# Performance work log

Measured on AMD Instinct MI355X. Metric: run time of the kernel, lower is better.

Reference implementation:

```python
import jax, jax.numpy as jnp
import numpy as np

N_HEAD = 4
GROUPS = 32
EPS = 1e-5


def group_norm(x, scale, bias):
    B, C, H, W = x.shape
    xg = x.reshape(B, GROUPS, C // GROUPS, H, W)
    mu = xg.mean(axis=(2, 3, 4), keepdims=True)
    var = xg.var(axis=(2, 3, 4), keepdims=True)
    xg = (xg - mu) * jax.lax.rsqrt(var + EPS)
    x = xg.reshape(B, C, H, W)
    return x * scale[None, :, None, None] + bias[None, :, None, None]


def setup_inputs() -> dict:
    key = jax.random.key(0)
    k0, k1, k2 = jax.random.split(key, 3)
    B, C, H, W = 2, 64, 64, 64
    x = jax.random.normal(k0, (B, C, H, W), dtype=jnp.float32)
    gn_scale = jnp.ones((C,), dtype=jnp.float32)
    gn_bias = jnp.zeros((C,), dtype=jnp.float32)
    w_qkv = jax.random.normal(k1, (3 * C, C), dtype=jnp.float32) * 0.05  # 1x1 conv, no bias
    w_out = jax.random.normal(k2, (C, C), dtype=jnp.float32) * 0.05     # 1x1 conv
    b_out = jnp.zeros((C,), dtype=jnp.float32)
    return {"x": x, "gn_scale": gn_scale, "gn_bias": gn_bias,
            "w_qkv": w_qkv, "w_out": w_out, "b_out": b_out}


def reference(x, gn_scale, gn_bias, w_qkv, w_out, b_out):
    B, C, H, W = x.shape
    head_dim = C // N_HEAD
    norm = group_norm(x, gn_scale, gn_bias)
    # 1x1 conv == channel matmul
    qkv = jnp.einsum('oc,bchw->bohw', w_qkv, norm)
    qkv = qkv.reshape(B, N_HEAD, head_dim * 3, H, W)
    q, k, v = jnp.split(qkv, 3, axis=2)  # each [B, n, head_dim, H, W]
    # full spatial attention scores, scaled by sqrt(channel) as in source
    attn = jnp.einsum('bnchw,bncyx->bnhwyx', q, k) / jnp.sqrt(jnp.float32(C))
    attn = jax.nn.softmax(attn.reshape(B, N_HEAD, H, W, H * W), axis=-1)
    attn = attn.reshape(B, N_HEAD, H, W, H, W)
    out = jnp.einsum('bnhwyx,bncyx->bnchw', attn, v).reshape(B, C, H, W)
    out = jnp.einsum('oc,bchw->bohw', w_out, out) + b_out[None, :, None, None]
    return out + x
```

## Files before the change

### kernel.cpp

```cpp
#include <hip/hip_runtime.h>
#include <hip/hip_bf16.h>

typedef __attribute__((ext_vector_type(8))) short short8;
typedef __attribute__((ext_vector_type(4))) float f32x4;
typedef __attribute__((ext_vector_type(16))) float f32x16;
typedef __attribute__((ext_vector_type(4))) unsigned short ushort4v;
typedef __attribute__((ext_vector_type(4))) unsigned int uint4v;

#define DEV static __device__ __forceinline__

DEV unsigned short f2bf(float f){
  unsigned u = __float_as_uint(f);
  u += 0x7fffu + ((u >> 16) & 1u);
  return (unsigned short)(u >> 16);
}

DEV unsigned pack2bf(float a, float b){
  __hip_bfloat162 h = __float22bfloat162_rn(make_float2(a, b));
  unsigned u;
  __builtin_memcpy(&u, &h, 4);
  return u;
}

#define QSCALE 0.180336880111f

__global__ __launch_bounds__(256) void gn_partial_k(const float* __restrict__ x,
                                                    float* __restrict__ gp){
  int blk = blockIdx.x;
  float4 v = ((const float4*)(x + (size_t)blk*1024))[threadIdx.x];
  float s = v.x+v.y+v.z+v.w;
  float q = v.x*v.x+v.y*v.y+v.z*v.z+v.w*v.w;
  #pragma unroll
  for (int off = 1; off < 64; off <<= 1){
    s += __shfl_xor(s, off);
    q += __shfl_xor(q, off);
  }
  __shared__ float red[8];
  int w = threadIdx.x >> 6;
  if ((threadIdx.x & 63) == 0){ red[w*2] = s; red[w*2+1] = q; }
  __syncthreads();
  if (threadIdx.x == 0){
    gp[blk*2+0] = red[0]+red[2]+red[4]+red[6];
    gp[blk*2+1] = red[1]+red[3]+red[5]+red[7];
  }
}

__global__ __launch_bounds__(256) void qkv_k(const float* __restrict__ x,
    const float* __restrict__ gp, const float* __restrict__ gsc,
    const float* __restrict__ gbi, const float* __restrict__ wq,
    unsigned short* __restrict__ q, unsigned short* __restrict__ k,
    unsigned short* __restrict__ v){
  int b  = blockIdx.x >> 7;
  int s0 = (blockIdx.x & 127) * 32;
  __shared__ float W[192][68];
  __shared__ float A[32][68];
  __shared__ float MS[32][2];
  int t = threadIdx.x;
  for (int i = t; i < 3072; i += 256){
    int o = i >> 4, c4 = (i & 15) * 4;
    *(float4*)&W[o][c4] = ((const float4*)wq)[i];
  }
  if (t < 32){
    float s = 0.f, ss = 0.f;
    #pragma unroll
    for (int i = 0; i < 8; ++i){
      const float* pp = gp + ((b*32 + t)*8 + i)*2;
      s += pp[0]; ss += pp[1];
    }
    float mean = s * (1.f/8192.f);
    MS[t][0] = mean;
    MS[t][1] = rsqrtf(ss * (1.f/8192.f) - mean*mean + 1e-5f);
  }
  __syncthreads();
  {
    int c  = t >> 2;
    int s8 = (t & 3) * 8;
    const float* px = x + ((size_t)b*64 + c)*4096 + s0 + s8;
    float4 v0 = *(const float4*)px;
    float4 v1 = *(const float4*)(px + 4);
    float sc = gsc[c] * MS[c>>1][1];
    float bi = gbi[c] - MS[c>>1][0] * sc;
    A[s8+0][c]=v0.x*sc+bi; A[s8+1][c]=v0.y*sc+bi; A[s8+2][c]=v0.z*sc+bi; A[s8+3][c]=v0.w*sc+bi;
    A[s8+4][c]=v1.x*sc+bi; A[s8+5][c]=v1.y*sc+bi; A[s8+6][c]=v1.z*sc+bi; A[s8+7][c]=v1.w*sc+bi;
  }
  __syncthreads();
  int sl = t >> 3, grp = t & 7;
  float acc[24];
  #pragma unroll
  for (int j = 0; j < 24; ++j) acc[j] = 0.f;
  for (int c4 = 0; c4 < 16; ++c4){
    float4 a = *(const float4*)&A[sl][c4*4];
    #pragma unroll
    for (int j = 0; j < 24; ++j){
      float4 wv = *(const float4*)&W[grp + j*8][c4*4];
      acc[j] = fmaf(a.x, wv.x, fmaf(a.y, wv.y, fmaf(a.z, wv.z, fmaf(a.w, wv.w, acc[j]))));
    }
  }
  int s = s0 + sl;
  #pragma unroll
  for (int j = 0; j < 24; ++j){
    int o = grp + j*8;
    int n = o / 48, r = o % 48;
    size_t base = (((size_t)b*4 + n)*4096 + s)*16;
    float val = acc[j];
    if (r < 16)       q[base + r]      = f2bf(val * QSCALE);
    else if (r < 32)  k[base + r - 16] = f2bf(val);
    else              v[base + r - 32] = f2bf(val);
  }
}

template<int LNSP>
__global__ __launch_bounds__(256) void attn_k(const unsigned short* __restrict__ qb,
    const unsigned short* __restrict__ kb, const unsigned short* __restrict__ vb,
    float* __restrict__ part, float* __restrict__ lsums){
  constexpr int NSP = 1 << LNSP;
  constexpr int NT  = 64 >> LNSP;
  int blk = blockIdx.x;
  int qt = blk & 31;
  int sp = (blk >> 5) & (NSP - 1);
  int bn = blk >> (5 + LNSP);
  int t = threadIdx.x, w = t >> 6, l = t & 63;
  int lq = l & 31, hi = l >> 5;

  const unsigned short* Kp = kb + ((size_t)bn*4096 + sp*(NT*64))*16;
  const unsigned short* Vp = vb + ((size_t)bn*4096 + sp*(NT*64))*16;
  int qrow = qt*128 + w*32;
  const unsigned short* Qp = qb + ((size_t)bn*4096 + qrow)*16;

  __shared__ alignas(16) unsigned short Vt[2][16][72];

  short8 qf = *(const short8*)(Qp + (size_t)lq*16 + hi*8);

  f32x16 O, zero;
  #pragma unroll
  for (int r = 0; r < 16; ++r){ O[r] = 0.f; zero[r] = 0.f; }

  short8 vones;
  #pragma unroll
  for (int r = 0; r < 8; ++r) vones[r] = (short)0x3F80;

  int skv = t >> 2, sd = (t & 3) * 4;
  int xk = skv & 15;
  int scol = (skv & 48) + (xk & 3) + (((xk >> 2) & 1) << 3) + (((xk >> 3) & 1) << 2);
  const unsigned short* vsrc = Vp + (size_t)skv*16 + sd;
  const unsigned short* kaddr = Kp + (size_t)lq*16 + hi*8;

  short8 kf0 = *(const short8*)(kaddr);
  short8 kf1 = *(const short8*)(kaddr + 512);
  {
    ushort4v vv = *(const ushort4v*)(vsrc);
    Vt[0][sd+0][scol]=vv[0]; Vt[0][sd+1][scol]=vv[1];
    Vt[0][sd+2][scol]=vv[2]; Vt[0][sd+3][scol]=vv[3];
  }

  for (int kt = 0; kt < NT; ++kt){
    __syncthreads();
    int cur = kt & 1;
    bool pf = (kt + 1) < NT;
    short8 kn0 = {}, kn1 = {};
    ushort4v vn = {};
    if (pf){
      const unsigned short* ka = kaddr + (size_t)(kt+1)*1024;
      kn0 = *(const short8*)(ka);
      kn1 = *(const short8*)(ka + 512);
      vn  = *(const ushort4v*)(vsrc + (size_t)(kt+1)*1024);
    }

    f32x16 sA = __builtin_amdgcn_mfma_f32_32x32x16_bf16(kf0, qf, zero, 0, 0, 0);
    f32x16 sB = __builtin_amdgcn_mfma_f32_32x32x16_bf16(kf1, qf, zero, 0, 0, 0);

    #pragma unroll
    for (int r = 0; r < 16; ++r) sA[r] = __builtin_amdgcn_exp2f(sA[r]);
    #pragma unroll
    for (int r = 0; r < 16; ++r) sB[r] = __builtin_amdgcn_exp2f(sB[r]);

    auto pvstep = [&](const f32x16& pc, int h8, int vcol){
      uint4v pw;
      pw[0] = pack2bf(pc[h8+0], pc[h8+1]);
      pw[1] = pack2bf(pc[h8+2], pc[h8+3]);
      pw[2] = pack2bf(pc[h8+4], pc[h8+5]);
      pw[3] = pack2bf(pc[h8+6], pc[h8+7]);
      short8 pa = __builtin_bit_cast(short8, pw);
      short8 vf = {};
      if (lq < 16)       vf = *(const short8*)(&Vt[cur][lq][vcol + hi*8]);
      else if (lq == 16) vf = vones;
      O = __builtin_amdgcn_mfma_f32_32x32x16_bf16(pa, vf, O, 0, 0, 0);
    };
    pvstep(sA, 0, 0);
    pvstep(sA, 8, 16);
    pvstep(sB, 0, 32);
    pvstep(sB, 8, 48);

    if (pf){
      Vt[cur^1][sd+0][scol]=vn[0]; Vt[cur^1][sd+1][scol]=vn[1];
      Vt[cur^1][sd+2][scol]=vn[2]; Vt[cur^1][sd+3][scol]=vn[3];
      kf0 = kn0; kf1 = kn1;
    }
  }

  float* Op = part + (((size_t)sp*8 + bn)*4096 + qrow)*16;
  size_t lbase = ((size_t)sp*8 + bn)*4096 + qrow;
  #pragma unroll
  for (int r = 0; r < 16; ++r){
    int qr = (r&3) + 8*(r>>2) + 4*hi;
    if (lq < 16) Op[(size_t)qr*16 + lq] = O[r];
  }
  if (lq == 16){
    #pragma unroll
    for (int r = 0; r < 16; ++r){
      int qr = (r&3) + 8*(r>>2) + 4*hi;
      lsums[lbase + qr] = O[r];
    }
  }
}

__global__ __launch_bounds__(256) void oproj_k(const float* __restrict__ part,
    const float* __restrict__ lsums, const float* __restrict__ wo,
    const float* __restrict__ bo, const float* __restrict__ x,
    float* __restrict__ out, int nsplit){
  int b  = blockIdx.x >> 8;
  int s0 = (blockIdx.x & 255) * 16;
  __shared__ float W[64][68];
  __shared__ float A[16][68];
  int t = threadIdx.x;
  for (int i = t; i < 1024; i += 256){
    int o = i >> 4, c4 = (i & 15) * 4;
    *(float4*)&W[o][c4] = ((const float4*)wo)[i];
  }
  {
    int sl = t & 15;
    int u  = t >> 4;
    int n = u >> 2, d4 = (u & 3) * 4;
    size_t row = ((size_t)b*4 + n)*4096 + s0 + sl;
    float L = 0.f;
    for (int sp = 0; sp < nsplit; ++sp) L += lsums[(size_t)sp*32768 + row];
    float4 acc = {0.f,0.f,0.f,0.f};
    for (int sp = 0; sp < nsplit; ++sp){
      float4 u0 = *(const float4*)(part + ((size_t)sp*32768 + row)*16 + d4);
      acc.x += u0.x; acc.y += u0.y; acc.z += u0.z; acc.w += u0.w;
    }
    float inv = 1.f / L;
    acc.x *= inv; acc.y *= inv; acc.z *= inv; acc.w *= inv;
    *(float4*)&A[sl][n*16 + d4] = acc;
  }
  __syncthreads();
  int sl = t & 15, grp = t >> 4;
  float acc[4] = {0.f,0.f,0.f,0.f};
  for (int c4 = 0; c4 < 16; ++c4){
    float4 a = *(const float4*)&A[sl][c4*4];
    #pragma unroll
    for (int j = 0; j < 4; ++j){
      float4 wv = *(const float4*)&W[grp + j*16][c4*4];
      acc[j] = fmaf(a.x, wv.x, fmaf(a.y, wv.y, fmaf(a.z, wv.z, fmaf(a.w, wv.w, acc[j]))));
    }
  }
  int s = s0 + sl;
  #pragma unroll
  for (int j = 0; j < 4; ++j){
    int o = grp + j*16;
    size_t idx = ((size_t)b*64 + o)*4096 + s;
    out[idx] = acc[j] + bo[o] + x[idx];
  }
}

extern "C" void kernel_launch(void* const* d_in, const int* in_sizes, int n_in,
                              void* d_out, int out_size, void* d_ws, size_t ws_size,
                              hipStream_t stream){
  const float* x   = (const float*)d_in[0];
  const float* gsc = (const float*)d_in[1];
  const float* gbi = (const float*)d_in[2];
  const float* wq  = (const float*)d_in[3];
  const float* wo  = (const float*)d_in[4];
  const float* bo  = (const float*)d_in[5];
  float* out = (float*)d_out;

  char* ws = (char*)d_ws;
  float* gp         = (float*)ws;
  unsigned short* q = (unsigned short*)(ws + 8192);
  unsigned short* k = (unsigned short*)(ws + 8192 + 1048576);
  unsigned short* v = (unsigned short*)(ws + 8192 + 2097152);
  float* part       = (float*)(ws + 8192 + 3145728);

  size_t need8 = 8192 + 3145728 + 8u*2097152 + 8u*131072;
  bool big = ws_size >= need8;
  int nsplit = big ? 8 : 4;
  float* lsums = (float*)(ws + 8192 + 3145728 + (size_t)nsplit*2097152);

  gn_partial_k<<<512,  256, 0, stream>>>(x, gp);
  qkv_k       <<<256,  256, 0, stream>>>(x, gp, gsc, gbi, wq, q, k, v);
  if (big) attn_k<3><<<2048, 256, 0, stream>>>(q, k, v, part, lsums);
  else     attn_k<2><<<1024, 256, 0, stream>>>(q, k, v, part, lsums);
  oproj_k     <<<512,  256, 0, stream>>>(part, lsums, wo, bo, x, out, nsplit);
}
```

Baseline: 61.71 us.

## Reorder attention block mapping, pad V tile with ones row, use nontemporal partials

Remaps block indices so batch-head varies fastest and query tile slowest, which changes L2 locality of K/V across concurrently running blocks. The V shared tile is enlarged to 32 rows with a constant ones row and zero padding, so every lane loads its MFMA operand from LDS instead of branching on the lane index. The V store into LDS moves to the top of the loop, before the barrier. Partial outputs and row sums are written and read with nontemporal hints to avoid polluting cache. The trade-offs are more LDS use, a one-time fill loop, and a barrier ordering that depends on the double-buffer indexing staying correct.

```diff
diff --git a/kernel.cpp b/kernel.cpp
--- a/kernel.cpp
+++ b/kernel.cpp
@@ -116,9 +116,9 @@
   constexpr int NSP = 1 << LNSP;
   constexpr int NT  = 64 >> LNSP;
   int blk = blockIdx.x;
-  int qt = blk & 31;
-  int sp = (blk >> 5) & (NSP - 1);
-  int bn = blk >> (5 + LNSP);
+  int bn = blk & 7;
+  int sp = (blk >> 3) & (NSP - 1);
+  int qt = blk >> (3 + LNSP);
   int t = threadIdx.x, w = t >> 6, l = t & 63;
   int lq = l & 31, hi = l >> 5;
 
@@ -127,17 +127,19 @@
   int qrow = qt*128 + w*32;
   const unsigned short* Qp = qb + ((size_t)bn*4096 + qrow)*16;
 
-  __shared__ alignas(16) unsigned short Vt[2][16][72];
+  __shared__ alignas(16) unsigned short Vt[2][32][72];
+  for (int i = t; i < 2304; i += 256){
+    int buf = (i >= 1152);
+    int ii  = buf ? i - 1152 : i;
+    int row = 16 + ii / 72, col = ii % 72;
+    Vt[buf][row][col] = (row == 16) ? (unsigned short)0x3F80 : (unsigned short)0;
+  }
 
   short8 qf = *(const short8*)(Qp + (size_t)lq*16 + hi*8);
 
   f32x16 O, zero;
   #pragma unroll
   for (int r = 0; r < 16; ++r){ O[r] = 0.f; zero[r] = 0.f; }
-
-  short8 vones;
-  #pragma unroll
-  for (int r = 0; r < 8; ++r) vones[r] = (short)0x3F80;
 
   int skv = t >> 2, sd = (t & 3) * 4;
   int xk = skv & 15;
@@ -147,15 +149,14 @@
 
   short8 kf0 = *(const short8*)(kaddr);
   short8 kf1 = *(const short8*)(kaddr + 512);
-  {
-    ushort4v vv = *(const ushort4v*)(vsrc);
-    Vt[0][sd+0][scol]=vv[0]; Vt[0][sd+1][scol]=vv[1];
-    Vt[0][sd+2][scol]=vv[2]; Vt[0][sd+3][scol]=vv[3];
-  }
+  ushort4v vv = *(const ushort4v*)(vsrc);
 
   for (int kt = 0; kt < NT; ++kt){
+    int cur = kt & 1;
+    Vt[cur][sd+0][scol]=vv[0]; Vt[cur][sd+1][scol]=vv[1];
+    Vt[cur][sd+2][scol]=vv[2]; Vt[cur][sd+3][scol]=vv[3];
     __syncthreads();
-    int cur = kt & 1;
+
     bool pf = (kt + 1) < NT;
     short8 kn0 = {}, kn1 = {};
     ushort4v vn = {};
@@ -181,9 +182,7 @@
       pw[2] = pack2bf(pc[h8+4], pc[h8+5]);
       pw[3] = pack2bf(pc[h8+6], pc[h8+7]);
       short8 pa = __builtin_bit_cast(short8, pw);
-      short8 vf = {};
-      if (lq < 16)       vf = *(const short8*)(&Vt[cur][lq][vcol + hi*8]);
-      else if (lq == 16) vf = vones;
+      short8 vf = *(const short8*)(&Vt[cur][lq][vcol + hi*8]);
       O = __builtin_amdgcn_mfma_f32_32x32x16_bf16(pa, vf, O, 0, 0, 0);
     };
     pvstep(sA, 0, 0);
@@ -191,11 +190,7 @@
     pvstep(sB, 0, 32);
     pvstep(sB, 8, 48);
 
-    if (pf){
-      Vt[cur^1][sd+0][scol]=vn[0]; Vt[cur^1][sd+1][scol]=vn[1];
-      Vt[cur^1][sd+2][scol]=vn[2]; Vt[cur^1][sd+3][scol]=vn[3];
-      kf0 = kn0; kf1 = kn1;
-    }
+    kf0 = kn0; kf1 = kn1; vv = vn;
   }
 
   float* Op = part + (((size_t)sp*8 + bn)*4096 + qrow)*16;
@@ -203,13 +198,13 @@
   #pragma unroll
   for (int r = 0; r < 16; ++r){
     int qr = (r&3) + 8*(r>>2) + 4*hi;
-    if (lq < 16) Op[(size_t)qr*16 + lq] = O[r];
+    if (lq < 16) __builtin_nontemporal_store(O[r], &Op[(size_t)qr*16 + lq]);
   }
   if (lq == 16){
     #pragma unroll
     for (int r = 0; r < 16; ++r){
       int qr = (r&3) + 8*(r>>2) + 4*hi;
-      lsums[lbase + qr] = O[r];
+      __builtin_nontemporal_store(O[r], &lsums[lbase + qr]);
     }
   }
 }
@@ -233,15 +228,17 @@
     int n = u >> 2, d4 = (u & 3) * 4;
     size_t row = ((size_t)b*4 + n)*4096 + s0 + sl;
     float L = 0.f;
-    for (int sp = 0; sp < nsplit; ++sp) L += lsums[(size_t)sp*32768 + row];
-    float4 acc = {0.f,0.f,0.f,0.f};
+    for (int sp = 0; sp < nsplit; ++sp)
+      L += __builtin_nontemporal_load(&lsums[(size_t)sp*32768 + row]);
+    f32x4 acc = {0.f,0.f,0.f,0.f};
     for (int sp = 0; sp < nsplit; ++sp){
-      float4 u0 = *(const float4*)(part + ((size_t)sp*32768 + row)*16 + d4);
-      acc.x += u0.x; acc.y += u0.y; acc.z += u0.z; acc.w += u0.w;
+      f32x4 u0 = __builtin_nontemporal_load(
+          (const f32x4*)(part + ((size_t)sp*32768 + row)*16 + d4));
+      acc += u0;
     }
     float inv = 1.f / L;
-    acc.x *= inv; acc.y *= inv; acc.z *= inv; acc.w *= inv;
-    *(float4*)&A[sl][n*16 + d4] = acc;
+    A[sl][n*16+d4+0] = acc[0]*inv; A[sl][n*16+d4+1] = acc[1]*inv;
+    A[sl][n*16+d4+2] = acc[2]*inv; A[sl][n*16+d4+3] = acc[3]*inv;
   }
   __syncthreads();
   int sl = t & 15, grp = t >> 4;
```

Result: no change. 60.70 us (-1.6%).
